# Kernel tuning notes

Hardware: AMD Instinct MI355X
Metric: run time of the kernel (lower is better)

Reference implementation:

```python
import jax, jax.numpy as jnp
import numpy as np

# ---- config (mirrors argparse-config of dnc_model) ----
T, B, IN = 64, 32, 64          # time-major input [T,B,IN]
N, Wd, R, NW = 512, 64, 4, 1   # memory_size, word_size, num_reads, num_writes
H, OUT = 256, 64               # controller hidden, output_size
CLIP = 20.0
EPS = 1e-6
IF = R*Wd + R + NW*Wd + NW + NW*Wd + NW*Wd + R + NW + NW + R*(1+2*NW)  # interface size = 471
CTRL_IN = IN + R*Wd


def setup_inputs() -> dict:
    key = jax.random.key(0)
    ks = jax.random.split(key, 6)
    g = lambda k, shape, s: (jax.random.normal(k, shape, jnp.float32) * s)
    return {
        "inputs": g(ks[0], (T, B, IN), 1.0),
        "Wx": g(ks[1], (CTRL_IN, 4*H), 0.05),
        "Wh": g(ks[2], (H, 4*H), 0.05),
        "b_lstm": jnp.zeros((4*H,), jnp.float32),
        "W_if": g(ks[3], (H, IF), 0.05),
        "b_if": jnp.zeros((IF,), jnp.float32),
        "W_out": g(ks[4], (H + R*Wd, OUT), 0.05),
        "b_out": jnp.zeros((OUT,), jnp.float32),
    }


def _clip(x):
    return jnp.clip(x, -CLIP, CLIP)


def _oneplus(x):
    return 1.0 + jax.nn.softplus(x)


def _content_weights(memory, keys, strengths):
    # memory [B,N,Wd], keys [B,K,Wd], strengths [B,K] -> softmax cosine weights [B,K,N]
    dot = jnp.einsum('bkw,bnw->bkn', keys, memory)
    mn = jnp.sqrt(jnp.sum(memory * memory, -1))          # [B,N]
    kn = jnp.sqrt(jnp.sum(keys * keys, -1))              # [B,K]
    sim = dot / (kn[..., None] * mn[:, None, :] + EPS)
    return jax.nn.softmax(sim * strengths[..., None], axis=-1)


def _allocation(usage):
    # usage [B,N] -> allocation weights [B,N] (sorted-free-list scheme)
    u = EPS + (1.0 - EPS) * usage
    idx = jnp.argsort(u, axis=-1)                        # ascending usage
    su = jnp.take_along_axis(u, idx, -1)
    cp = jnp.cumprod(su, axis=-1)
    excl = jnp.concatenate([jnp.ones_like(cp[:, :1]), cp[:, :-1]], -1)
    a_sorted = (1.0 - su) * excl
    inv = jnp.argsort(idx, axis=-1)
    return jnp.take_along_axis(a_sorted, inv, -1)


def _dnc_forward(inputs, Wx, Wh, b_lstm, W_if, b_if, W_out, b_out):
    eye = jnp.eye(N, dtype=inputs.dtype)

    def step(carry, x_t):
        h, c, mem, rw, ww_prev, link, prec, usage, reads = carry
        # ---- controller LSTM (prev read vectors fed in) ----
        ctrl_in = jnp.concatenate([x_t, reads.reshape(B, R*Wd)], -1)
        gates = ctrl_in @ Wx + h @ Wh + b_lstm
        ig, fg, gg, og = jnp.split(gates, 4, -1)
        c = jax.nn.sigmoid(fg) * c + jax.nn.sigmoid(ig) * jnp.tanh(gg)
        h = jax.nn.sigmoid(og) * jnp.tanh(c)
        hc, cc = _clip(h), _clip(c)
        # ---- interface vector ----
        itf = hc @ W_if + b_if
        off = 0
        read_keys = itf[:, off:off+R*Wd].reshape(B, R, Wd); off += R*Wd
        read_str = _oneplus(itf[:, off:off+R]); off += R
        write_keys = itf[:, off:off+NW*Wd].reshape(B, NW, Wd); off += NW*Wd
        write_str = _oneplus(itf[:, off:off+NW]); off += NW
        erase = jax.nn.sigmoid(itf[:, off:off+NW*Wd]).reshape(B, NW, Wd); off += NW*Wd
        write_vecs = itf[:, off:off+NW*Wd].reshape(B, NW, Wd); off += NW*Wd
        free_g = jax.nn.sigmoid(itf[:, off:off+R]); off += R
        alloc_g = jax.nn.sigmoid(itf[:, off:off+NW]); off += NW
        write_g = jax.nn.sigmoid(itf[:, off:off+NW]); off += NW
        modes = jax.nn.softmax(itf[:, off:off+R*(1+2*NW)].reshape(B, R, 1+2*NW), -1)
        bwd_mode = modes[..., :NW]
        fwd_mode = modes[..., NW:2*NW]
        content_mode = modes[..., 2*NW]
        # ---- usage update (uses prev write/read weights) ----
        u = usage + (1.0 - usage) * (1.0 - jnp.prod(1.0 - ww_prev, axis=1))
        psi = jnp.prod(1.0 - free_g[..., None] * rw, axis=1)
        usage = u * psi
        # ---- write weights: allocation + content ----
        allocs = []
        u_run = usage
        for hd in range(NW):
            a = _allocation(u_run)
            allocs.append(a)
            u_run = u_run + (1.0 - u_run) * (write_g[:, hd:hd+1] * alloc_g[:, hd:hd+1]) * a
        alloc = jnp.stack(allocs, 1)                      # [B,NW,N]
        wc = _content_weights(mem, write_keys, write_str) # [B,NW,N]
        ww = write_g[..., None] * (alloc_g[..., None] * alloc + (1.0 - alloc_g[..., None]) * wc)
        # ---- erase / add write ----
        erase_w = ww[..., None] * erase[:, :, None, :]    # [B,NW,N,Wd]
        mem = mem * jnp.prod(1.0 - erase_w, axis=1) + jnp.einsum('bhn,bhw->bnw', ww, write_vecs)
        # ---- temporal link + precedence ----
        w_i = ww[..., :, None]
        w_j = ww[..., None, :]
        link = (1.0 - w_i - w_j) * link + w_i * prec[..., None, :]
        link = link * (1.0 - eye)
        prec = (1.0 - ww.sum(-1, keepdims=True)) * prec + ww
        # ---- read weights: content + forward/backward linkage ----
        rc = _content_weights(mem, read_keys, read_str)   # [B,R,N]
        fw = jnp.einsum('bhij,brj->brhi', link, rw)       # forward  [B,R,NW,N]
        bw = jnp.einsum('bhji,brj->brhi', link, rw)       # backward [B,R,NW,N]
        rw = (content_mode[..., None] * rc
              + jnp.einsum('brh,brhn->brn', fwd_mode, fw)
              + jnp.einsum('brh,brhn->brn', bwd_mode, bw))
        reads = jnp.einsum('brn,bnw->brw', rw, mem)       # [B,R,Wd]
        out = _clip(jnp.concatenate([hc, reads.reshape(B, R*Wd)], -1) @ W_out + b_out)
        return (hc, cc, mem, rw, ww, link, prec, usage, reads), out

    z = jnp.zeros
    dt = inputs.dtype
    carry0 = (z((B, H), dt), z((B, H), dt), z((B, N, Wd), dt), z((B, R, N), dt),
              z((B, NW, N), dt), z((B, NW, N, N), dt), z((B, NW, N), dt),
              z((B, N), dt), z((B, R, Wd), dt))
    _, outs = jax.lax.scan(step, carry0, inputs)
    return outs  # [T, B, OUT]


def reference(inputs, Wx, Wh, b_lstm, W_if, b_if, W_out, b_out):
    return _dnc_forward(inputs, Wx, Wh, b_lstm, W_if, b_if, W_out, b_out)
```

## Files before the change

kernel.cpp:

```cpp
#include <hip/hip_runtime.h>
#include <math.h>

#define Tn 64
#define Bn 32
#define INn 64
#define Nn 512
#define WDn 64
#define Rn 4
#define Hn 256
#define G4H 1024
#define OUTn 64
#define IFn 471
#define CLIPV 20.0f
#define EPSV 1e-6f

#define OFF_RKEY 0
#define OFF_RSTR 256
#define OFF_WKEY 260
#define OFF_WSTR 324
#define OFF_ERASE 325
#define OFF_WVEC 389
#define OFF_FREE 453
#define OFF_AG 457
#define OFF_WG 458
#define OFF_MODES 459

__device__ float S_h[2][Bn][Hn];
__device__ float S_c[2][Bn][Hn];
__device__ float S_gates[2][Bn][G4H];
__device__ float S_mem[Bn][Nn][WDn];
__device__ float S_rw[Bn][Rn][Nn];
__device__ float S_ww[2][Bn][Nn];
__device__ float S_link[Bn][Nn][Nn];
__device__ float S_prec[2][Bn][Nn];
__device__ float S_usage[2][Bn][Nn];
__device__ float S_reads[Bn][Rn][WDn];
__device__ float S_itf[Bn][IFn];
__device__ float S_fw[Bn][Rn][Nn];
__device__ float S_bwp[Bn][8][Rn*Nn];
__device__ float S_sumww[Bn];
__device__ unsigned int g_hh[16];
__device__ unsigned int g_ww[Bn][16];
__device__ unsigned int g_ld[Bn][16];
__device__ unsigned int g_fin[16];

__device__ __forceinline__ float sigm(float x){ return 1.f/(1.f+expf(-x)); }
__device__ __forceinline__ float clipv(float x){ return fminf(fmaxf(x,-CLIPV),CLIPV); }
__device__ __forceinline__ float oneplusf(float x){
  float sp = (x > 0.f) ? (x + log1pf(expf(-x))) : log1pf(expf(x));
  return 1.f + sp;
}
__device__ __forceinline__ float wredsum(float v){
  #pragma unroll
  for (int o=32;o>0;o>>=1) v += __shfl_xor(v,o,64);
  return v;
}
__device__ __forceinline__ float bredsum(float v, volatile float* scr){
  v = wredsum(v);
  if ((threadIdx.x & 63) == 0) scr[threadIdx.x >> 6] = v;
  __syncthreads();
  float s = scr[0];
  #pragma unroll
  for (int i=1;i<8;i++) s += scr[i];
  __syncthreads();
  return s;
}
__device__ __forceinline__ float bredmax(float v, volatile float* scr){
  #pragma unroll
  for (int o=32;o>0;o>>=1) v = fmaxf(v,__shfl_xor(v,o,64));
  if ((threadIdx.x & 63) == 0) scr[threadIdx.x >> 6] = v;
  __syncthreads();
  float m = scr[0];
  #pragma unroll
  for (int i=1;i<8;i++) m = fmaxf(m, scr[i]);
  __syncthreads();
  return m;
}
__device__ __forceinline__ void sig_release(unsigned int* flag){
  __builtin_amdgcn_fence(__ATOMIC_RELEASE, "agent");
  __hip_atomic_fetch_add(flag, 1u, __ATOMIC_RELAXED, __HIP_MEMORY_SCOPE_AGENT);
}
__device__ __forceinline__ void spin_until(unsigned int* flag, unsigned int target){
  while (__hip_atomic_load(flag, __ATOMIC_RELAXED, __HIP_MEMORY_SCOPE_AGENT) < target)
    __builtin_amdgcn_s_sleep(4);
}
__device__ __forceinline__ void wait_acq1(unsigned int* f, unsigned int tgt){
  if (threadIdx.x==0){
    spin_until(f, tgt);
    __builtin_amdgcn_fence(__ATOMIC_ACQUIRE, "agent");
  }
  __syncthreads();
}

extern "C" __global__ void __launch_bounds__(256)
k_init(){
  size_t g = (size_t)blockIdx.x*256 + threadIdx.x;
  size_t stride = (size_t)gridDim.x*256;
  float* lk = &S_link[0][0][0];
  for (size_t i=g; i<(size_t)Bn*Nn*Nn; i+=stride) lk[i]=0.f;
  float* mm = &S_mem[0][0][0];
  for (size_t i=g; i<(size_t)Bn*Nn*WDn; i+=stride) mm[i]=0.f;
  float* rr = &S_rw[0][0][0];
  for (size_t i=g; i<(size_t)Bn*Rn*Nn; i+=stride) rr[i]=0.f;
  float* rd = &S_reads[0][0][0];
  for (size_t i=g; i<(size_t)Bn*Rn*WDn; i+=stride) rd[i]=0.f;
  for (size_t i=g; i<(size_t)2*Bn*Nn; i+=stride){
    S_ww[0][0][i]=0.f; S_prec[0][0][i]=0.f; S_usage[0][0][i]=0.f;
  }
  for (size_t i=g; i<(size_t)2*Bn*Hn; i+=stride){
    S_h[0][0][i]=0.f; S_c[0][0][i]=0.f;
  }
  if (blockIdx.x==0){
    for (int i=threadIdx.x; i<16; i+=256){ g_hh[i]=0u; g_fin[i]=0u; }
    for (int i=threadIdx.x; i<Bn*16; i+=256){
      ((unsigned int*)g_ww)[i]=0u; ((unsigned int*)g_ld)[i]=0u;
    }
  }
}

struct ShG { float ctrl[Bn][65]; };
struct ShA {
  float hc[Hn];
  float itf[IFn];
  unsigned long long keys[Nn];
  float alloc[Nn];
  float sim[Nn];
  float tile[64][65];
  float wkey[WDn];
  float red[8];
  float knw;
};
struct ShL {
  float ww[Nn];
  float prec[Nn];
  float rw[Rn][Nn];
  float bwp4[4][Rn][Nn];
};
struct ShF {
  float er[WDn];
  float wv[WDn];
  float rk[Rn][WDn];
  float betar[Rn];
  float knr[Rn];
  float modes[Rn][4];
  float ww[Nn];
  float tile[64][65];
  float rsim[Rn][Nn];
  float fw[Rn][Nn];
  float bw[Rn][Nn];
  float part[8][Rn][WDn];
  float vin[512];
  float red[8];
};
union ShU { ShA a; ShL l; ShF f; ShG g; };

extern "C" __global__ void __launch_bounds__(512)
k_gates_pro(const float* __restrict__ xin, const float* __restrict__ Wx,
            const float* __restrict__ Wh, const float* __restrict__ b_lstm){
  __shared__ ShG sg;
  const int tid = threadIdx.x, lane = tid & 63, wvi = tid >> 6;
  const int j = blockIdx.x*64 + lane;
  const int b0 = wvi*4;
  float bias = b_lstm[j];
  float a0=bias, a1=bias, a2=bias, a3=bias;
  for (int c=0;c<9;++c){
    #pragma unroll
    for (int u=0;u<4;u++){
      int e = u*512 + tid;
      int b2 = e >> 6, kk = e & 63;
      float v;
      if (c==0)       v = xin[(size_t)b2*INn + kk];
      else if (c<5)   v = 0.f;
      else            v = 0.f;
      sg.ctrl[b2][kk] = v;
    }
    __syncthreads();
    const float* wb = (c<5) ? (Wx + (size_t)(c*64)*G4H + j)
                            : (Wh + (size_t)((c-5)*64)*G4H + j);
    #pragma unroll
    for (int kk=0;kk<64;kk++){
      float wv = wb[(size_t)kk*G4H];
      a0 += sg.ctrl[b0+0][kk]*wv;
      a1 += sg.ctrl[b0+1][kk]*wv;
      a2 += sg.ctrl[b0+2][kk]*wv;
      a3 += sg.ctrl[b0+3][kk]*wv;
    }
    __syncthreads();
  }
  S_gates[0][b0+0][j]=a0;
  S_gates[0][b0+1][j]=a1;
  S_gates[0][b0+2][j]=a2;
  S_gates[0][b0+3][j]=a3;
}

extern "C" __global__ void __launch_bounds__(512, 4)
k_step(int t, const float* __restrict__ xin,
       const float* __restrict__ Wx, const float* __restrict__ Wh,
       const float* __restrict__ b_lstm,
       const float* __restrict__ W_if, const float* __restrict__ b_if,
       const float* __restrict__ W_out, const float* __restrict__ b_out,
       float* __restrict__ outp){
  __shared__ ShU sh;
  const int tid = threadIdx.x;
  const int lane = tid & 63, wvi = tid >> 6;
  const int bid = blockIdx.x;
  const int cur = t&1, prev = cur^1;

  if (bid < 32){
    const int b = bid;
    if (tid < Hn){
      int h = tid;
      float g0=S_gates[cur][b][h],     g1=S_gates[cur][b][Hn+h];
      float g2=S_gates[cur][b][2*Hn+h],g3=S_gates[cur][b][3*Hn+h];
      float cold = S_c[prev][b][h];
      float cn = sigm(g1)*cold + sigm(g0)*tanhf(g2);
      float hn = sigm(g3)*tanhf(cn);
      float hcv = clipv(hn);
      S_c[cur][b][h] = clipv(cn);
      S_h[cur][b][h] = hcv;
      sh.a.hc[h] = hcv;
    }
    __syncthreads();
    if (tid==0) sig_release(&g_hh[0]);
    if (tid < IFn){
      float acc = b_if[tid];
      for (int k=0;k<Hn;k+=16){
        float s = 0.f;
        #pragma unroll
        for (int u=0;u<16;u++) s += sh.a.hc[k+u]*W_if[(size_t)(k+u)*IFn + tid];
        acc += s;
      }
      sh.a.itf[tid] = acc;
      S_itf[b][tid] = acc;
    }
    __syncthreads();
    if (tid < WDn) sh.a.wkey[tid] = sh.a.itf[OFF_WKEY+tid];
    {
      float fg0=sigm(sh.a.itf[OFF_FREE+0]), fg1=sigm(sh.a.itf[OFF_FREE+1]);
      float fg2=sigm(sh.a.itf[OFF_FREE+2]), fg3=sigm(sh.a.itf[OFF_FREE+3]);
      int n = tid;
      float uu = S_usage[prev][b][n], wwp = S_ww[prev][b][n];
      float u = uu + (1.f-uu)*wwp;
      float psi = (1.f - fg0*S_rw[b][0][n])*(1.f - fg1*S_rw[b][1][n])
                * (1.f - fg2*S_rw[b][2][n])*(1.f - fg3*S_rw[b][3][n]);
      float un = u*psi;
      S_usage[cur][b][n] = un;
      float v = EPSV + (1.f-EPSV)*un;
      sh.a.keys[n] = ((unsigned long long)__float_as_uint(v) << 32) | (unsigned)n;
    }
    __syncthreads();
    if (wvi==0){
      float kv = sh.a.wkey[lane];
      float s2 = wredsum(kv*kv);
      if (lane==0) sh.a.knw = sqrtf(s2);
    }
    {
      unsigned long long myk = sh.a.keys[tid];
      float prod = 1.f;
      for (int j=0;j<Nn;j+=8){
        #pragma unroll
        for (int u=0;u<8;u++){
          unsigned long long kj = sh.a.keys[j+u];
          float uj = __uint_as_float((unsigned)(kj>>32));
          prod *= (kj < myk) ? uj : 1.f;
        }
      }
      float myu = __uint_as_float((unsigned)(myk>>32));
      sh.a.alloc[tid] = (1.f - myu)*prod;
    }
    __syncthreads();
    float betaw = oneplusf(sh.a.itf[OFF_WSTR]);
    for (int tile=0;tile<8;tile++){
      #pragma unroll
      for (int u=0;u<8;u++){
        int e = u*512 + tid;
        int nn = e>>6, w = e&63;
        sh.a.tile[nn][w] = S_mem[b][tile*64+nn][w];
      }
      __syncthreads();
      {
        int nn = tid>>3, qq = tid&7;
        float d=0.f, nrm=0.f;
        #pragma unroll
        for (int i=0;i<8;i++){
          int w = qq*8+i;
          float m = sh.a.tile[nn][w];
          d += m*sh.a.wkey[w]; nrm += m*m;
        }
        #pragma unroll
        for (int o=1;o<8;o<<=1){ d += __shfl_xor(d,o,64); nrm += __shfl_xor(nrm,o,64); }
        if (qq==0){
          int n = tile*64+nn;
          sh.a.sim[n] = betaw * d / (sh.a.knw*sqrtf(nrm) + EPSV);
        }
      }
      __syncthreads();
    }
    {
      float v = sh.a.sim[tid];
      float mx = bredmax(v, sh.a.red);
      float e = expf(v - mx);
      float ssum = bredsum(e, sh.a.red);
      float wc = e/ssum;
      float ag = sigm(sh.a.itf[OFF_AG]);
      float wg = sigm(sh.a.itf[OFF_WG]);
      float wwv = wg*(ag*sh.a.alloc[tid] + (1.f-ag)*wc);
      S_ww[cur][b][tid] = wwv;
      float wsum = bredsum(wwv, sh.a.red);
      if (tid==0) S_sumww[b] = wsum;
    }
    __syncthreads();
    if (tid==0) sig_release(&g_ww[b][0]);

  } else if (bid < 288){
    const int idx = bid - 32;
    const int b = idx >> 3, ch = idx & 7;
    const int i0 = ch*64;
    wait_acq1(&g_ww[b][0], (unsigned)(t+1));
    sh.l.ww[tid]   = S_ww[cur][b][tid];
    sh.l.prec[tid] = S_prec[prev][b][tid];
    for (int k=tid;k<Rn*Nn;k+=512) ((float*)sh.l.rw)[k] = ((const float*)S_rw[b])[k];
    __syncthreads();
    float sumww = S_sumww[b];
    float wj[2][4], pj[2][4], rj[4][2][4];
    #pragma unroll
    for (int jjc=0;jjc<2;jjc++){
      float4 w4 = ((const float4*)sh.l.ww)[jjc*64+lane];
      float4 p4 = ((const float4*)sh.l.prec)[jjc*64+lane];
      wj[jjc][0]=w4.x; wj[jjc][1]=w4.y; wj[jjc][2]=w4.z; wj[jjc][3]=w4.w;
      pj[jjc][0]=p4.x; pj[jjc][1]=p4.y; pj[jjc][2]=p4.z; pj[jjc][3]=p4.w;
      #pragma unroll
      for (int r=0;r<4;r++){
        float4 r4 = ((const float4*)sh.l.rw[r])[jjc*64+lane];
        rj[r][jjc][0]=r4.x; rj[r][jjc][1]=r4.y; rj[r][jjc][2]=r4.z; rj[r][jjc][3]=r4.w;
      }
    }
    float bwa[4][2][4];
    #pragma unroll
    for (int r=0;r<4;r++)
      #pragma unroll
      for (int jjc=0;jjc<2;jjc++)
        #pragma unroll
        for (int s=0;s<4;s++) bwa[r][jjc][s]=0.f;
    for (int rr=0;rr<8;rr++){
      const int i = i0 + wvi*8 + rr;
      float wi = sh.l.ww[i];
      float ci = 1.f - wi;
      float ri[4] = {sh.l.rw[0][i], sh.l.rw[1][i], sh.l.rw[2][i], sh.l.rw[3][i]};
      float f[4] = {0.f,0.f,0.f,0.f};
      float4* lrow4 = (float4*)(&S_link[b][i][0]);
      #pragma unroll
      for (int jjc=0;jjc<2;jjc++){
        float4 L4 = lrow4[jjc*64+lane];
        float Ls[4] = {L4.x, L4.y, L4.z, L4.w};
        #pragma unroll
        for (int s=0;s<4;s++){
          float Ln = (ci - wj[jjc][s])*Ls[s] + wi*pj[jjc][s];
          int j = jjc*256 + lane*4 + s;
          Ln = (j==i) ? 0.f : Ln;
          Ls[s] = Ln;
          #pragma unroll
          for (int r=0;r<4;r++){
            f[r] += Ln*rj[r][jjc][s];
            bwa[r][jjc][s] += Ln*ri[r];
          }
        }
        float4 Lo; Lo.x=Ls[0]; Lo.y=Ls[1]; Lo.z=Ls[2]; Lo.w=Ls[3];
        lrow4[jjc*64+lane] = Lo;
      }
      #pragma unroll
      for (int r=0;r<4;r++){
        float fr = wredsum(f[r]);
        if (lane==0) S_fw[b][r][i] = fr;
      }
    }
    if (wvi < 4){
      #pragma unroll
      for (int r=0;r<4;r++)
        #pragma unroll
        for (int jjc=0;jjc<2;jjc++){
          float4 v4; v4.x=bwa[r][jjc][0]; v4.y=bwa[r][jjc][1]; v4.z=bwa[r][jjc][2]; v4.w=bwa[r][jjc][3];
          ((float4*)sh.l.bwp4[wvi][r])[jjc*64+lane] = v4;
        }
    }
    __syncthreads();
    if (wvi >= 4){
      int v = wvi-4;
      #pragma unroll
      for (int r=0;r<4;r++)
        #pragma unroll
        for (int jjc=0;jjc<2;jjc++){
          float4 v4 = ((float4*)sh.l.bwp4[v][r])[jjc*64+lane];
          v4.x+=bwa[r][jjc][0]; v4.y+=bwa[r][jjc][1]; v4.z+=bwa[r][jjc][2]; v4.w+=bwa[r][jjc][3];
          ((float4*)sh.l.bwp4[v][r])[jjc*64+lane] = v4;
        }
    }
    __syncthreads();
    for (int k=tid;k<Rn*Nn;k+=512){
      float s = ((float*)sh.l.bwp4[0])[k] + ((float*)sh.l.bwp4[1])[k]
              + ((float*)sh.l.bwp4[2])[k] + ((float*)sh.l.bwp4[3])[k];
      S_bwp[b][ch][k] = s;
    }
    if (tid < 64){
      int j = i0 + tid;
      S_prec[cur][b][j] = (1.f - sumww)*sh.l.prec[j] + sh.l.ww[j];
    }
    __syncthreads();
    if (tid==0) sig_release(&g_ld[b][0]);

  } else if (bid < 320){
    const int b = bid - 288;
    wait_acq1(&g_ww[b][0], (unsigned)(t+1));
    if (tid < WDn){
      sh.f.er[tid] = sigm(S_itf[b][OFF_ERASE+tid]);
      sh.f.wv[tid] = S_itf[b][OFF_WVEC+tid];
    } else if (tid < WDn + Rn*WDn){
      int k2 = tid - WDn;
      sh.f.rk[k2>>6][k2&63] = S_itf[b][OFF_RKEY + k2];
    } else if (tid < WDn + Rn*WDn + Rn){
      int r = tid - (WDn+Rn*WDn);
      sh.f.betar[r] = oneplusf(S_itf[b][OFF_RSTR + r]);
    } else if (tid >= 384 && tid < 384+Rn){
      int r = tid - 384;
      float m0 = S_itf[b][OFF_MODES + r*3 + 0];
      float m1 = S_itf[b][OFF_MODES + r*3 + 1];
      float m2 = S_itf[b][OFF_MODES + r*3 + 2];
      float mx = fmaxf(m0,fmaxf(m1,m2));
      float e0=expf(m0-mx), e1=expf(m1-mx), e2=expf(m2-mx);
      float si = e0+e1+e2;
      sh.f.modes[r][0]=e0/si; sh.f.modes[r][1]=e1/si; sh.f.modes[r][2]=e2/si;
    }
    sh.f.ww[tid] = S_ww[cur][b][tid];
    __syncthreads();
    if (wvi < 4){
      float kv = sh.f.rk[wvi][lane];
      float s2 = wredsum(kv*kv);
      if (lane==0) sh.f.knr[wvi] = sqrtf(s2);
    }
    for (int tile=0;tile<8;tile++){
      #pragma unroll
      for (int u=0;u<8;u++){
        int e = u*512 + tid;
        int nn = e>>6, w = e&63;
        int n = tile*64+nn;
        float m = S_mem[b][n][w];
        float wwn = sh.f.ww[n];
        m = m*(1.f - wwn*sh.f.er[w]) + wwn*sh.f.wv[w];
        S_mem[b][n][w] = m;
        sh.f.tile[nn][w] = m;
      }
      __syncthreads();
      {
        int nn = tid>>3, qq = tid&7;
        float a0=0.f,a1=0.f,a2=0.f,a3=0.f,nrm=0.f;
        #pragma unroll
        for (int i=0;i<8;i++){
          int w = qq*8+i;
          float m = sh.f.tile[nn][w];
          a0 += m*sh.f.rk[0][w]; a1 += m*sh.f.rk[1][w];
          a2 += m*sh.f.rk[2][w]; a3 += m*sh.f.rk[3][w];
          nrm += m*m;
        }
        #pragma unroll
        for (int o=1;o<8;o<<=1){
          a0 += __shfl_xor(a0,o,64); a1 += __shfl_xor(a1,o,64);
          a2 += __shfl_xor(a2,o,64); a3 += __shfl_xor(a3,o,64);
          nrm += __shfl_xor(nrm,o,64);
        }
        if (qq==0){
          int n = tile*64+nn;
          float mn = sqrtf(nrm);
          sh.f.rsim[0][n] = sh.f.betar[0]*a0/(sh.f.knr[0]*mn + EPSV);
          sh.f.rsim[1][n] = sh.f.betar[1]*a1/(sh.f.knr[1]*mn + EPSV);
          sh.f.rsim[2][n] = sh.f.betar[2]*a2/(sh.f.knr[2]*mn + EPSV);
          sh.f.rsim[3][n] = sh.f.betar[3]*a3/(sh.f.knr[3]*mn + EPSV);
        }
      }
      __syncthreads();
    }
    for (int r=0;r<Rn;r++){
      float v = sh.f.rsim[r][tid];
      float mx = bredmax(v, sh.f.red);
      float e = expf(v - mx);
      float ssum = bredsum(e, sh.f.red);
      sh.f.rsim[r][tid] = e/ssum;
    }
    __syncthreads();
    wait_acq1(&g_ld[b][0], 8u*(unsigned)(t+1));
    for (int k=tid;k<Rn*Nn;k+=512){
      ((float*)sh.f.fw)[k] = ((const float*)S_fw[b])[k];
      float sbw = 0.f;
      #pragma unroll
      for (int ch=0;ch<8;ch++) sbw += S_bwp[b][ch][k];
      ((float*)sh.f.bw)[k] = sbw;
    }
    __syncthreads();
    for (int k=tid;k<Rn*Nn;k+=512){
      int r = k>>9, n = k&511;
      float v = sh.f.modes[r][2]*sh.f.rsim[r][n] + sh.f.modes[r][1]*sh.f.fw[r][n]
              + sh.f.modes[r][0]*sh.f.bw[r][n];
      sh.f.rsim[r][n] = v;
      S_rw[b][r][n] = v;
    }
    __syncthreads();
    {
      float a0=0.f,a1=0.f,a2=0.f,a3=0.f;
      #pragma unroll 4
      for (int nn=0;nn<64;nn++){
        int n = wvi*64+nn;
        float m = S_mem[b][n][lane];
        a0 += sh.f.rsim[0][n]*m; a1 += sh.f.rsim[1][n]*m;
        a2 += sh.f.rsim[2][n]*m; a3 += sh.f.rsim[3][n]*m;
      }
      sh.f.part[wvi][0][lane]=a0; sh.f.part[wvi][1][lane]=a1;
      sh.f.part[wvi][2][lane]=a2; sh.f.part[wvi][3][lane]=a3;
    }
    __syncthreads();
    if (tid < 256){
      int r = tid>>6, w = tid&63;
      float sv = 0.f;
      #pragma unroll
      for (int v=0;v<8;v++) sv += sh.f.part[v][r][w];
      S_reads[b][r][w] = sv;
      sh.f.vin[256+tid] = sv;
      sh.f.vin[tid] = S_h[cur][b][tid];
    }
    __syncthreads();
    {
      int qq = tid>>6, o = tid&63;
      float sacc = 0.f;
      for (int k2=qq*64;k2<qq*64+64;k2+=8){
        #pragma unroll
        for (int u=0;u<8;u++) sacc += sh.f.vin[k2+u]*W_out[(size_t)(k2+u)*OUTn + o];
      }
      sh.f.part[qq][0][o] = sacc;
    }
    __syncthreads();
    if (tid < 64){
      float sv = b_out[tid];
      #pragma unroll
      for (int qq=0;qq<8;qq++) sv += sh.f.part[qq][0][tid];
      outp[((size_t)t*Bn + b)*OUTn + tid] = clipv(sv);
    }
    __syncthreads();
    if (tid==0) sig_release(&g_fin[0]);

  } else {
    if (t+1 >= Tn) return;
    const int jt = bid - 320;
    const int j = jt*64 + lane;
    const int b0 = wvi*4;
    const int hp = cur;
    float bias = b_lstm[j];
    float a0=bias, a1=bias, a2=bias, a3=bias;
    wait_acq1(&g_hh[0], 32u*(unsigned)(t+1));
    for (int c=0;c<5;++c){
      #pragma unroll
      for (int u=0;u<4;u++){
        int e = u*512 + tid;
        int b2 = e >> 6, kk = e & 63;
        float v;
        if (c==0) v = xin[((size_t)(t+1)*Bn + b2)*INn + kk];
        else      v = S_h[hp][b2][(c-1)*64 + kk];
        sh.g.ctrl[b2][kk] = v;
      }
      __syncthreads();
      const float* wb = (c==0) ? (Wx + j)
                               : (Wh + (size_t)((c-1)*64)*G4H + j);
      #pragma unroll
      for (int kk=0;kk<64;kk++){
        float wv = wb[(size_t)kk*G4H];
        a0 += sh.g.ctrl[b0+0][kk]*wv;
        a1 += sh.g.ctrl[b0+1][kk]*wv;
        a2 += sh.g.ctrl[b0+2][kk]*wv;
        a3 += sh.g.ctrl[b0+3][kk]*wv;
      }
      __syncthreads();
    }
    wait_acq1(&g_fin[0], 32u*(unsigned)(t+1));
    for (int c=0;c<4;++c){
      #pragma unroll
      for (int u=0;u<4;u++){
        int e = u*512 + tid;
        int b2 = e >> 6, kk = e & 63;
        sh.g.ctrl[b2][kk] = ((const float*)S_reads[b2])[c*64 + kk];
      }
      __syncthreads();
      const float* wb = Wx + (size_t)(INn + c*64)*G4H + j;
      #pragma unroll
      for (int kk=0;kk<64;kk++){
        float wv = wb[(size_t)kk*G4H];
        a0 += sh.g.ctrl[b0+0][kk]*wv;
        a1 += sh.g.ctrl[b0+1][kk]*wv;
        a2 += sh.g.ctrl[b0+2][kk]*wv;
        a3 += sh.g.ctrl[b0+3][kk]*wv;
      }
      __syncthreads();
    }
    const int gs = (t+1)&1;
    S_gates[gs][b0+0][j]=a0;
    S_gates[gs][b0+1][j]=a1;
    S_gates[gs][b0+2][j]=a2;
    S_gates[gs][b0+3][j]=a3;
  }
}

extern "C" void kernel_launch(void* const* d_in, const int* in_sizes, int n_in,
                              void* d_out, int out_size, void* d_ws, size_t ws_size,
                              hipStream_t stream){
  (void)in_sizes; (void)n_in; (void)d_ws; (void)ws_size; (void)out_size;
  const float* xin = (const float*)d_in[0];
  const float* Wx  = (const float*)d_in[1];
  const float* Wh  = (const float*)d_in[2];
  const float* bl  = (const float*)d_in[3];
  const float* Wif = (const float*)d_in[4];
  const float* bif = (const float*)d_in[5];
  const float* Wo  = (const float*)d_in[6];
  const float* bo  = (const float*)d_in[7];
  hipLaunchKernelGGL(k_init, dim3(1024), dim3(256), 0, stream);
  hipLaunchKernelGGL(k_gates_pro, dim3(16), dim3(512), 0, stream, xin, Wx, Wh, bl);
  for (int t=0; t<Tn; ++t){
    hipLaunchKernelGGL(k_step, dim3(336), dim3(512), 0, stream,
                       t, xin, Wx, Wh, bl, Wif, bif, Wo, bo, (float*)d_out);
  }
}
```

Baseline: 6.347 ms.

## Split interface matmul and write-content sim across link blocks, merge final stage

Moves the per-batch interface projection and write-key content similarity out of the single per-batch block into the 8 link blocks per batch, with new per-batch flags (g_hb, g_itf, g_sim) to hand results back. The former final-stage blocks (memory update, read content, read vectors, output) are merged into the per-batch allocation block, so the grid drops from 336 to 304 blocks. The prologue gate kernel also stops multiplying by zero inputs, and the spin sleep is shortened. The goal is to shorten the serial critical path per step, at the cost of more cross-block handshakes and a longer per-batch block.

```diff
diff --git a/kernel.cpp b/kernel.cpp
--- a/kernel.cpp
+++ b/kernel.cpp
@@ -36,10 +36,14 @@
 __device__ float S_usage[2][Bn][Nn];
 __device__ float S_reads[Bn][Rn][WDn];
 __device__ float S_itf[Bn][IFn];
+__device__ float S_wsim[Bn][Nn];
 __device__ float S_fw[Bn][Rn][Nn];
 __device__ float S_bwp[Bn][8][Rn*Nn];
 __device__ float S_sumww[Bn];
 __device__ unsigned int g_hh[16];
+__device__ unsigned int g_hb[Bn][16];
+__device__ unsigned int g_itf[Bn][16];
+__device__ unsigned int g_sim[Bn][16];
 __device__ unsigned int g_ww[Bn][16];
 __device__ unsigned int g_ld[Bn][16];
 __device__ unsigned int g_fin[16];
@@ -82,7 +86,7 @@
 }
 __device__ __forceinline__ void spin_until(unsigned int* flag, unsigned int target){
   while (__hip_atomic_load(flag, __ATOMIC_RELAXED, __HIP_MEMORY_SCOPE_AGENT) < target)
-    __builtin_amdgcn_s_sleep(4);
+    __builtin_amdgcn_s_sleep(1);
 }
 __device__ __forceinline__ void wait_acq1(unsigned int* f, unsigned int tgt){
   if (threadIdx.x==0){
@@ -113,46 +117,43 @@
   if (blockIdx.x==0){
     for (int i=threadIdx.x; i<16; i+=256){ g_hh[i]=0u; g_fin[i]=0u; }
     for (int i=threadIdx.x; i<Bn*16; i+=256){
-      ((unsigned int*)g_ww)[i]=0u; ((unsigned int*)g_ld)[i]=0u;
+      ((unsigned int*)g_hb)[i]=0u; ((unsigned int*)g_itf)[i]=0u;
+      ((unsigned int*)g_sim)[i]=0u; ((unsigned int*)g_ww)[i]=0u;
+      ((unsigned int*)g_ld)[i]=0u;
     }
   }
 }
 
 struct ShG { float ctrl[Bn][65]; };
-struct ShA {
-  float hc[Hn];
+struct ShAF {
   float itf[IFn];
-  unsigned long long keys[Nn];
-  float alloc[Nn];
-  float sim[Nn];
-  float tile[64][65];
-  float wkey[WDn];
+  float ww[Nn];
   float red[8];
-  float knw;
+  float betar[Rn], knr[Rn], modes[Rn][4];
+  float er[WDn], wv[WDn], rk[Rn][WDn];
+  union {
+    struct { unsigned long long keys[Nn]; float alloc[Nn]; float wsim[Nn]; } pre;
+    struct {
+      float tile[64][65];
+      float rsim[Rn][Nn];
+      float fw[Rn][Nn];
+      float bw[Rn][Nn];
+      float part[8][Rn][WDn];
+      float vin[512];
+    } post;
+  } u;
 };
 struct ShL {
+  float hc[Hn];
+  float ipart[8][64];
+  float wkey[WDn];
+  float knw, betaw;
   float ww[Nn];
   float prec[Nn];
   float rw[Rn][Nn];
   float bwp4[4][Rn][Nn];
 };
-struct ShF {
-  float er[WDn];
-  float wv[WDn];
-  float rk[Rn][WDn];
-  float betar[Rn];
-  float knr[Rn];
-  float modes[Rn][4];
-  float ww[Nn];
-  float tile[64][65];
-  float rsim[Rn][Nn];
-  float fw[Rn][Nn];
-  float bw[Rn][Nn];
-  float part[8][Rn][WDn];
-  float vin[512];
-  float red[8];
-};
-union ShU { ShA a; ShL l; ShF f; ShG g; };
+union ShU { ShAF a; ShL l; ShG g; };
 
 extern "C" __global__ void __launch_bounds__(512)
 k_gates_pro(const float* __restrict__ xin, const float* __restrict__ Wx,
@@ -163,20 +164,15 @@
   const int b0 = wvi*4;
   float bias = b_lstm[j];
   float a0=bias, a1=bias, a2=bias, a3=bias;
-  for (int c=0;c<9;++c){
+  {
     #pragma unroll
     for (int u=0;u<4;u++){
       int e = u*512 + tid;
       int b2 = e >> 6, kk = e & 63;
-      float v;
-      if (c==0)       v = xin[(size_t)b2*INn + kk];
-      else if (c<5)   v = 0.f;
-      else            v = 0.f;
-      sg.ctrl[b2][kk] = v;
-    }
-    __syncthreads();
-    const float* wb = (c<5) ? (Wx + (size_t)(c*64)*G4H + j)
-                            : (Wh + (size_t)((c-5)*64)*G4H + j);
+      sg.ctrl[b2][kk] = xin[(size_t)b2*INn + kk];
+    }
+    __syncthreads();
+    const float* wb = Wx + j;
     #pragma unroll
     for (int kk=0;kk<64;kk++){
       float wv = wb[(size_t)kk*G4H];
@@ -185,7 +181,6 @@
       a2 += sg.ctrl[b0+2][kk]*wv;
       a3 += sg.ctrl[b0+3][kk]*wv;
     }
-    __syncthreads();
   }
   S_gates[0][b0+0][j]=a0;
   S_gates[0][b0+1][j]=a1;
@@ -215,26 +210,33 @@
       float cold = S_c[prev][b][h];
       float cn = sigm(g1)*cold + sigm(g0)*tanhf(g2);
       float hn = sigm(g3)*tanhf(cn);
-      float hcv = clipv(hn);
       S_c[cur][b][h] = clipv(cn);
-      S_h[cur][b][h] = hcv;
-      sh.a.hc[h] = hcv;
-    }
-    __syncthreads();
-    if (tid==0) sig_release(&g_hh[0]);
-    if (tid < IFn){
-      float acc = b_if[tid];
-      for (int k=0;k<Hn;k+=16){
-        float s = 0.f;
-        #pragma unroll
-        for (int u=0;u<16;u++) s += sh.a.hc[k+u]*W_if[(size_t)(k+u)*IFn + tid];
-        acc += s;
-      }
-      sh.a.itf[tid] = acc;
-      S_itf[b][tid] = acc;
-    }
-    __syncthreads();
-    if (tid < WDn) sh.a.wkey[tid] = sh.a.itf[OFF_WKEY+tid];
+      S_h[cur][b][h] = clipv(hn);
+    }
+    __syncthreads();
+    if (tid==0){ sig_release(&g_hb[b][0]); sig_release(&g_hh[0]); }
+    wait_acq1(&g_itf[b][0], 8u*(unsigned)(t+1));
+    for (int k=tid;k<IFn;k+=512) sh.a.itf[k] = S_itf[b][k];
+    __syncthreads();
+    if (tid < WDn){
+      sh.a.er[tid] = sigm(sh.a.itf[OFF_ERASE+tid]);
+      sh.a.wv[tid] = sh.a.itf[OFF_WVEC+tid];
+    } else if (tid < WDn + Rn*WDn){
+      int k2 = tid - WDn;
+      sh.a.rk[k2>>6][k2&63] = sh.a.itf[OFF_RKEY + k2];
+    } else if (tid < WDn + Rn*WDn + Rn){
+      int r = tid - (WDn+Rn*WDn);
+      sh.a.betar[r] = oneplusf(sh.a.itf[OFF_RSTR + r]);
+    } else if (tid >= 384 && tid < 384+Rn){
+      int r = tid - 384;
+      float m0 = sh.a.itf[OFF_MODES + r*3 + 0];
+      float m1 = sh.a.itf[OFF_MODES + r*3 + 1];
+      float m2 = sh.a.itf[OFF_MODES + r*3 + 2];
+      float mx = fmaxf(m0,fmaxf(m1,m2));
+      float e0=expf(m0-mx), e1=expf(m1-mx), e2=expf(m2-mx);
+      float si = e0+e1+e2;
+      sh.a.modes[r][0]=e0/si; sh.a.modes[r][1]=e1/si; sh.a.modes[r][2]=e2/si;
+    }
     {
       float fg0=sigm(sh.a.itf[OFF_FREE+0]), fg1=sigm(sh.a.itf[OFF_FREE+1]);
       float fg2=sigm(sh.a.itf[OFF_FREE+2]), fg3=sigm(sh.a.itf[OFF_FREE+3]);
@@ -246,76 +248,214 @@
       float un = u*psi;
       S_usage[cur][b][n] = un;
       float v = EPSV + (1.f-EPSV)*un;
-      sh.a.keys[n] = ((unsigned long long)__float_as_uint(v) << 32) | (unsigned)n;
-    }
-    __syncthreads();
-    if (wvi==0){
-      float kv = sh.a.wkey[lane];
+      sh.a.u.pre.keys[n] = ((unsigned long long)__float_as_uint(v) << 32) | (unsigned)n;
+    }
+    __syncthreads();
+    if (wvi < 4){
+      float kv = sh.a.rk[wvi][lane];
       float s2 = wredsum(kv*kv);
-      if (lane==0) sh.a.knw = sqrtf(s2);
+      if (lane==0) sh.a.knr[wvi] = sqrtf(s2);
     }
     {
-      unsigned long long myk = sh.a.keys[tid];
+      unsigned long long myk = sh.a.u.pre.keys[tid];
       float prod = 1.f;
       for (int j=0;j<Nn;j+=8){
         #pragma unroll
         for (int u=0;u<8;u++){
-          unsigned long long kj = sh.a.keys[j+u];
+          unsigned long long kj = sh.a.u.pre.keys[j+u];
           float uj = __uint_as_float((unsigned)(kj>>32));
           prod *= (kj < myk) ? uj : 1.f;
         }
       }
       float myu = __uint_as_float((unsigned)(myk>>32));
-      sh.a.alloc[tid] = (1.f - myu)*prod;
-    }
-    __syncthreads();
-    float betaw = oneplusf(sh.a.itf[OFF_WSTR]);
-    for (int tile=0;tile<8;tile++){
-      #pragma unroll
-      for (int u=0;u<8;u++){
-        int e = u*512 + tid;
-        int nn = e>>6, w = e&63;
-        sh.a.tile[nn][w] = S_mem[b][tile*64+nn][w];
-      }
-      __syncthreads();
-      {
-        int nn = tid>>3, qq = tid&7;
-        float d=0.f, nrm=0.f;
-        #pragma unroll
-        for (int i=0;i<8;i++){
-          int w = qq*8+i;
-          float m = sh.a.tile[nn][w];
-          d += m*sh.a.wkey[w]; nrm += m*m;
-        }
-        #pragma unroll
-        for (int o=1;o<8;o<<=1){ d += __shfl_xor(d,o,64); nrm += __shfl_xor(nrm,o,64); }
-        if (qq==0){
-          int n = tile*64+nn;
-          sh.a.sim[n] = betaw * d / (sh.a.knw*sqrtf(nrm) + EPSV);
-        }
-      }
-      __syncthreads();
-    }
+      sh.a.u.pre.alloc[tid] = (1.f - myu)*prod;
+    }
+    wait_acq1(&g_sim[b][0], 8u*(unsigned)(t+1));
+    sh.a.u.pre.wsim[tid] = S_wsim[b][tid];
+    __syncthreads();
     {
-      float v = sh.a.sim[tid];
+      float v = sh.a.u.pre.wsim[tid];
       float mx = bredmax(v, sh.a.red);
       float e = expf(v - mx);
       float ssum = bredsum(e, sh.a.red);
       float wc = e/ssum;
       float ag = sigm(sh.a.itf[OFF_AG]);
       float wg = sigm(sh.a.itf[OFF_WG]);
-      float wwv = wg*(ag*sh.a.alloc[tid] + (1.f-ag)*wc);
+      float wwv = wg*(ag*sh.a.u.pre.alloc[tid] + (1.f-ag)*wc);
       S_ww[cur][b][tid] = wwv;
+      sh.a.ww[tid] = wwv;
       float wsum = bredsum(wwv, sh.a.red);
       if (tid==0) S_sumww[b] = wsum;
     }
     __syncthreads();
     if (tid==0) sig_release(&g_ww[b][0]);
+    for (int tile=0;tile<8;tile++){
+      #pragma unroll
+      for (int u=0;u<8;u++){
+        int e = u*512 + tid;
+        int nn = e>>6, w = e&63;
+        int n = tile*64+nn;
+        float m = S_mem[b][n][w];
+        float wwn = sh.a.ww[n];
+        m = m*(1.f - wwn*sh.a.er[w]) + wwn*sh.a.wv[w];
+        S_mem[b][n][w] = m;
+        sh.a.u.post.tile[nn][w] = m;
+      }
+      __syncthreads();
+      {
+        int nn = tid>>3, qq = tid&7;
+        float a0=0.f,a1=0.f,a2=0.f,a3=0.f,nrm=0.f;
+        #pragma unroll
+        for (int i=0;i<8;i++){
+          int w = qq*8+i;
+          float m = sh.a.u.post.tile[nn][w];
+          a0 += m*sh.a.rk[0][w]; a1 += m*sh.a.rk[1][w];
+          a2 += m*sh.a.rk[2][w]; a3 += m*sh.a.rk[3][w];
+          nrm += m*m;
+        }
+        #pragma unroll
+        for (int o=1;o<8;o<<=1){
+          a0 += __shfl_xor(a0,o,64); a1 += __shfl_xor(a1,o,64);
+          a2 += __shfl_xor(a2,o,64); a3 += __shfl_xor(a3,o,64);
+          nrm += __shfl_xor(nrm,o,64);
+        }
+        if (qq==0){
+          int n = tile*64+nn;
+          float mn = sqrtf(nrm);
+          sh.a.u.post.rsim[0][n] = sh.a.betar[0]*a0/(sh.a.knr[0]*mn + EPSV);
+          sh.a.u.post.rsim[1][n] = sh.a.betar[1]*a1/(sh.a.knr[1]*mn + EPSV);
+          sh.a.u.post.rsim[2][n] = sh.a.betar[2]*a2/(sh.a.knr[2]*mn + EPSV);
+          sh.a.u.post.rsim[3][n] = sh.a.betar[3]*a3/(sh.a.knr[3]*mn + EPSV);
+        }
+      }
+      __syncthreads();
+    }
+    for (int r=0;r<Rn;r++){
+      float v = sh.a.u.post.rsim[r][tid];
+      float mx = bredmax(v, sh.a.red);
+      float e = expf(v - mx);
+      float ssum = bredsum(e, sh.a.red);
+      sh.a.u.post.rsim[r][tid] = e/ssum;
+    }
+    __syncthreads();
+    wait_acq1(&g_ld[b][0], 8u*(unsigned)(t+1));
+    for (int k=tid;k<Rn*Nn;k+=512){
+      ((float*)sh.a.u.post.fw)[k] = ((const float*)S_fw[b])[k];
+      float sbw = 0.f;
+      #pragma unroll
+      for (int ch=0;ch<8;ch++) sbw += S_bwp[b][ch][k];
+      ((float*)sh.a.u.post.bw)[k] = sbw;
+    }
+    __syncthreads();
+    for (int k=tid;k<Rn*Nn;k+=512){
+      int r = k>>9, n = k&511;
+      float v = sh.a.modes[r][2]*sh.a.u.post.rsim[r][n]
+              + sh.a.modes[r][1]*sh.a.u.post.fw[r][n]
+              + sh.a.modes[r][0]*sh.a.u.post.bw[r][n];
+      sh.a.u.post.rsim[r][n] = v;
+      S_rw[b][r][n] = v;
+    }
+    __syncthreads();
+    {
+      float a0=0.f,a1=0.f,a2=0.f,a3=0.f;
+      #pragma unroll 4
+      for (int nn=0;nn<64;nn++){
+        int n = wvi*64+nn;
+        float m = S_mem[b][n][lane];
+        a0 += sh.a.u.post.rsim[0][n]*m; a1 += sh.a.u.post.rsim[1][n]*m;
+        a2 += sh.a.u.post.rsim[2][n]*m; a3 += sh.a.u.post.rsim[3][n]*m;
+      }
+      sh.a.u.post.part[wvi][0][lane]=a0; sh.a.u.post.part[wvi][1][lane]=a1;
+      sh.a.u.post.part[wvi][2][lane]=a2; sh.a.u.post.part[wvi][3][lane]=a3;
+    }
+    __syncthreads();
+    if (tid < 256){
+      int r = tid>>6, w = tid&63;
+      float sv = 0.f;
+      #pragma unroll
+      for (int v=0;v<8;v++) sv += sh.a.u.post.part[v][r][w];
+      S_reads[b][r][w] = sv;
+      sh.a.u.post.vin[256+tid] = sv;
+      sh.a.u.post.vin[tid] = S_h[cur][b][tid];
+    }
+    __syncthreads();
+    {
+      int qq = tid>>6, o = tid&63;
+      float sacc = 0.f;
+      for (int k2=qq*64;k2<qq*64+64;k2+=8){
+        #pragma unroll
+        for (int u=0;u<8;u++) sacc += sh.a.u.post.vin[k2+u]*W_out[(size_t)(k2+u)*OUTn + o];
+      }
+      sh.a.u.post.part[qq][0][o] = sacc;
+    }
+    __syncthreads();
+    if (tid < 64){
+      float sv = b_out[tid];
+      #pragma unroll
+      for (int qq=0;qq<8;qq++) sv += sh.a.u.post.part[qq][0][tid];
+      outp[((size_t)t*Bn + b)*OUTn + tid] = clipv(sv);
+    }
+    __syncthreads();
+    if (tid==0) sig_release(&g_fin[0]);
 
   } else if (bid < 288){
     const int idx = bid - 32;
     const int b = idx >> 3, ch = idx & 7;
     const int i0 = ch*64;
+    wait_acq1(&g_hb[b][0], (unsigned)(t+1));
+    if (tid < Hn) sh.l.hc[tid] = S_h[cur][b][tid];
+    __syncthreads();
+    const int col0 = ch*59;
+    const int ncol = (col0+59 <= IFn) ? 59 : (IFn - col0);
+    {
+      float acc = 0.f;
+      if (lane < ncol){
+        const float* wp = W_if + (size_t)(wvi*32)*IFn + col0 + lane;
+        #pragma unroll
+        for (int kk=0;kk<32;kk++)
+          acc += sh.l.hc[wvi*32+kk]*wp[(size_t)kk*IFn];
+      }
+      sh.l.ipart[wvi][lane] = acc;
+    }
+    __syncthreads();
+    if (tid < ncol){
+      float s = b_if[col0+tid];
+      #pragma unroll
+      for (int w=0;w<8;w++) s += sh.l.ipart[w][tid];
+      S_itf[b][col0+tid] = s;
+    }
+    __syncthreads();
+    if (tid==0) sig_release(&g_itf[b][0]);
+    wait_acq1(&g_itf[b][0], 8u*(unsigned)(t+1));
+    if (tid < WDn) sh.l.wkey[tid] = S_itf[b][OFF_WKEY+tid];
+    else if (tid==64) sh.l.betaw = oneplusf(S_itf[b][OFF_WSTR]);
+    __syncthreads();
+    if (wvi==0){
+      float kv = sh.l.wkey[lane];
+      float s2 = wredsum(kv*kv);
+      if (lane==0) sh.l.knw = sqrtf(s2);
+    }
+    __syncthreads();
+    {
+      int nn = tid>>3, qq = tid&7;
+      int n = i0 + nn;
+      const float4* mp = (const float4*)(&S_mem[b][n][qq*8]);
+      float4 ma = mp[0], mb = mp[1];
+      float d, nrm;
+      {
+        float k0=sh.l.wkey[qq*8+0], k1=sh.l.wkey[qq*8+1], k2=sh.l.wkey[qq*8+2], k3=sh.l.wkey[qq*8+3];
+        float k4=sh.l.wkey[qq*8+4], k5=sh.l.wkey[qq*8+5], k6=sh.l.wkey[qq*8+6], k7=sh.l.wkey[qq*8+7];
+        d   = ma.x*k0+ma.y*k1+ma.z*k2+ma.w*k3 + mb.x*k4+mb.y*k5+mb.z*k6+mb.w*k7;
+        nrm = ma.x*ma.x+ma.y*ma.y+ma.z*ma.z+ma.w*ma.w
+            + mb.x*mb.x+mb.y*mb.y+mb.z*mb.z+mb.w*mb.w;
+      }
+      #pragma unroll
+      for (int o=1;o<8;o<<=1){ d += __shfl_xor(d,o,64); nrm += __shfl_xor(nrm,o,64); }
+      if (qq==0)
+        S_wsim[b][n] = sh.l.betaw * d / (sh.l.knw*sqrtf(nrm) + EPSV);
+    }
+    __syncthreads();
+    if (tid==0) sig_release(&g_sim[b][0]);
     wait_acq1(&g_ww[b][0], (unsigned)(t+1));
     sh.l.ww[tid]   = S_ww[cur][b][tid];
     sh.l.prec[tid] = S_prec[prev][b][tid];
@@ -408,146 +548,9 @@
     __syncthreads();
     if (tid==0) sig_release(&g_ld[b][0]);
 
-  } else if (bid < 320){
-    const int b = bid - 288;
-    wait_acq1(&g_ww[b][0], (unsigned)(t+1));
-    if (tid < WDn){
-      sh.f.er[tid] = sigm(S_itf[b][OFF_ERASE+tid]);
-      sh.f.wv[tid] = S_itf[b][OFF_WVEC+tid];
-    } else if (tid < WDn + Rn*WDn){
-      int k2 = tid - WDn;
-      sh.f.rk[k2>>6][k2&63] = S_itf[b][OFF_RKEY + k2];
-    } else if (tid < WDn + Rn*WDn + Rn){
-      int r = tid - (WDn+Rn*WDn);
-      sh.f.betar[r] = oneplusf(S_itf[b][OFF_RSTR + r]);
-    } else if (tid >= 384 && tid < 384+Rn){
-      int r = tid - 384;
-      float m0 = S_itf[b][OFF_MODES + r*3 + 0];
-      float m1 = S_itf[b][OFF_MODES + r*3 + 1];
-      float m2 = S_itf[b][OFF_MODES + r*3 + 2];
-      float mx = fmaxf(m0,fmaxf(m1,m2));
-      float e0=expf(m0-mx), e1=expf(m1-mx), e2=expf(m2-mx);
-      float si = e0+e1+e2;
-      sh.f.modes[r][0]=e0/si; sh.f.modes[r][1]=e1/si; sh.f.modes[r][2]=e2/si;
-    }
-    sh.f.ww[tid] = S_ww[cur][b][tid];
-    __syncthreads();
-    if (wvi < 4){
-      float kv = sh.f.rk[wvi][lane];
-      float s2 = wredsum(kv*kv);
-      if (lane==0) sh.f.knr[wvi] = sqrtf(s2);
-    }
-    for (int tile=0;tile<8;tile++){
-      #pragma unroll
-      for (int u=0;u<8;u++){
-        int e = u*512 + tid;
-        int nn = e>>6, w = e&63;
-        int n = tile*64+nn;
-        float m = S_mem[b][n][w];
-        float wwn = sh.f.ww[n];
-        m = m*(1.f - wwn*sh.f.er[w]) + wwn*sh.f.wv[w];
-        S_mem[b][n][w] = m;
-        sh.f.tile[nn][w] = m;
-      }
-      __syncthreads();
-      {
-        int nn = tid>>3, qq = tid&7;
-        float a0=0.f,a1=0.f,a2=0.f,a3=0.f,nrm=0.f;
-        #pragma unroll
-        for (int i=0;i<8;i++){
-          int w = qq*8+i;
-          float m = sh.f.tile[nn][w];
-          a0 += m*sh.f.rk[0][w]; a1 += m*sh.f.rk[1][w];
-          a2 += m*sh.f.rk[2][w]; a3 += m*sh.f.rk[3][w];
-          nrm += m*m;
-        }
-        #pragma unroll
-        for (int o=1;o<8;o<<=1){
-          a0 += __shfl_xor(a0,o,64); a1 += __shfl_xor(a1,o,64);
-          a2 += __shfl_xor(a2,o,64); a3 += __shfl_xor(a3,o,64);
-          nrm += __shfl_xor(nrm,o,64);
-        }
-        if (qq==0){
-          int n = tile*64+nn;
-          float mn = sqrtf(nrm);
-          sh.f.rsim[0][n] = sh.f.betar[0]*a0/(sh.f.knr[0]*mn + EPSV);
-          sh.f.rsim[1][n] = sh.f.betar[1]*a1/(sh.f.knr[1]*mn + EPSV);
-          sh.f.rsim[2][n] = sh.f.betar[2]*a2/(sh.f.knr[2]*mn + EPSV);
-          sh.f.rsim[3][n] = sh.f.betar[3]*a3/(sh.f.knr[3]*mn + EPSV);
-        }
-      }
-      __syncthreads();
-    }
-    for (int r=0;r<Rn;r++){
-      float v = sh.f.rsim[r][tid];
-      float mx = bredmax(v, sh.f.red);
-      float e = expf(v - mx);
-      float ssum = bredsum(e, sh.f.red);
-      sh.f.rsim[r][tid] = e/ssum;
-    }
-    __syncthreads();
-    wait_acq1(&g_ld[b][0], 8u*(unsigned)(t+1));
-    for (int k=tid;k<Rn*Nn;k+=512){
-      ((float*)sh.f.fw)[k] = ((const float*)S_fw[b])[k];
-      float sbw = 0.f;
-      #pragma unroll
-      for (int ch=0;ch<8;ch++) sbw += S_bwp[b][ch][k];
-      ((float*)sh.f.bw)[k] = sbw;
-    }
-    __syncthreads();
-    for (int k=tid;k<Rn*Nn;k+=512){
-      int r = k>>9, n = k&511;
-      float v = sh.f.modes[r][2]*sh.f.rsim[r][n] + sh.f.modes[r][1]*sh.f.fw[r][n]
-              + sh.f.modes[r][0]*sh.f.bw[r][n];
-      sh.f.rsim[r][n] = v;
-      S_rw[b][r][n] = v;
-    }
-    __syncthreads();
-    {
-      float a0=0.f,a1=0.f,a2=0.f,a3=0.f;
-      #pragma unroll 4
-      for (int nn=0;nn<64;nn++){
-        int n = wvi*64+nn;
-        float m = S_mem[b][n][lane];
-        a0 += sh.f.rsim[0][n]*m; a1 += sh.f.rsim[1][n]*m;
-        a2 += sh.f.rsim[2][n]*m; a3 += sh.f.rsim[3][n]*m;
-      }
-      sh.f.part[wvi][0][lane]=a0; sh.f.part[wvi][1][lane]=a1;
-      sh.f.part[wvi][2][lane]=a2; sh.f.part[wvi][3][lane]=a3;
-    }
-    __syncthreads();
-    if (tid < 256){
-      int r = tid>>6, w = tid&63;
-      float sv = 0.f;
-      #pragma unroll
-      for (int v=0;v<8;v++) sv += sh.f.part[v][r][w];
-      S_reads[b][r][w] = sv;
-      sh.f.vin[256+tid] = sv;
-      sh.f.vin[tid] = S_h[cur][b][tid];
-    }
-    __syncthreads();
-    {
-      int qq = tid>>6, o = tid&63;
-      float sacc = 0.f;
-      for (int k2=qq*64;k2<qq*64+64;k2+=8){
-        #pragma unroll
-        for (int u=0;u<8;u++) sacc += sh.f.vin[k2+u]*W_out[(size_t)(k2+u)*OUTn + o];
-      }
-      sh.f.part[qq][0][o] = sacc;
-    }
-    __syncthreads();
-    if (tid < 64){
-      float sv = b_out[tid];
-      #pragma unroll
-      for (int qq=0;qq<8;qq++) sv += sh.f.part[qq][0][tid];
-      outp[((size_t)t*Bn + b)*OUTn + tid] = clipv(sv);
-    }
-    __syncthreads();
-    if (tid==0) sig_release(&g_fin[0]);
-
   } else {
     if (t+1 >= Tn) return;
-    const int jt = bid - 320;
+    const int jt = bid - 288;
     const int j = jt*64 + lane;
     const int b0 = wvi*4;
     const int hp = cur;
@@ -620,7 +623,7 @@
   hipLaunchKernelGGL(k_init, dim3(1024), dim3(256), 0, stream);
   hipLaunchKernelGGL(k_gates_pro, dim3(16), dim3(512), 0, stream, xin, Wx, Wh, bl);
   for (int t=0; t<Tn; ++t){
-    hipLaunchKernelGGL(k_step, dim3(336), dim3(512), 0, stream,
+    hipLaunchKernelGGL(k_step, dim3(304), dim3(512), 0, stream,
                        t, xin, Wx, Wh, bl, Wif, bif, Wo, bo, (float*)d_out);
   }
 }
```

New measurement: 6.271 ms. No clear change (-1.2%).
